# Kernel optimization log

Measured on AMD Instinct MI355X. Metric: run time of the kernel, lower is better.

The kernel has to match this reference:

```python
import jax, jax.numpy as jnp
import numpy as np

N_NODES = 8192
N_FEATURES = 512
EMB = 128
N_HEADS = 4
EPS = 1e-6


def setup_inputs() -> dict:
    key = jax.random.key(0)
    k1, k2, k3 = jax.random.split(key, 3)
    X = jax.random.normal(k1, (N_NODES, N_FEATURES), dtype=jnp.float32)
    W = jax.random.normal(k2, (N_FEATURES, EMB), dtype=jnp.float32)
    Z = jax.random.normal(k3, (N_HEADS, N_NODES, EMB), dtype=jnp.float32)
    beta = jnp.ones((), dtype=jnp.float32)
    return {"X": X, "W": W, "Z": Z, "beta": beta}


def reference(X, W, Z, beta):
    # DenseLayer: node embedding
    X_emb = X @ W                                   # [N, E]
    # AffinityLayer: Z @ X_emb^T then cosine-style normalization
    aff = jnp.einsum('hne,me->hnm', Z, X_emb)       # [H, N, N]
    X_norm = jnp.linalg.norm(X_emb, axis=-1)        # [N]
    Z_norm = jnp.linalg.norm(Z, axis=-1)            # [H, N]
    aff = aff / (X_norm[None, None, :] + EPS)
    aff = aff / (Z_norm[:, :, None] + EPS)
    # PoolingLayer: max over heads
    aff = jnp.max(aff, axis=0)                      # [N, N]
    # undirected -> symmetrize
    aff = (aff + aff.T) / 2.0
    # ScalingLayer: map [-1,1] -> [0,1]
    aff = (aff + 1.0) / 2.0
    # ExponentiationLayer
    aff = jnp.power(aff, beta)
    return aff
```

## Files before the change

kernel.cpp:

```cpp
#include <hip/hip_runtime.h>
#include <stdint.h>

#define N_NODES 8192
#define N_FEAT  512
#define EMB     128
#define N_HEADS 4
#define TILE    64
#define TGRID   (N_NODES / TILE)

typedef __attribute__((ext_vector_type(8))) short bf16x8;
typedef __attribute__((ext_vector_type(4))) float f32x4;

__device__ __forceinline__ unsigned short f2bf(float f) {
  union { float f; unsigned int u; } x; x.f = f;
  unsigned int r = (x.u + 0x7FFFu + ((x.u >> 16) & 1u)) >> 16;
  return (unsigned short)r;
}

__global__ void __launch_bounds__(256) xw_kernel(const float* __restrict__ X,
                                                 const float* __restrict__ W,
                                                 float* __restrict__ Xe) {
  __shared__ float xs[8][N_FEAT];
  const int t = threadIdx.x;
  const int row0 = blockIdx.x * 8;
#pragma unroll
  for (int i = 0; i < 16; ++i) {
    int idx = t + i * 256;
    xs[idx >> 9][idx & 511] = X[(size_t)(row0 + (idx >> 9)) * N_FEAT + (idx & 511)];
  }
  __syncthreads();
  const int j = t & 127;
  const int rh = t >> 7;
  float a0 = 0.f, a1 = 0.f, a2 = 0.f, a3 = 0.f;
  for (int k = 0; k < N_FEAT; k += 4) {
    float w0 = W[(k + 0) * EMB + j];
    float w1 = W[(k + 1) * EMB + j];
    float w2 = W[(k + 2) * EMB + j];
    float w3 = W[(k + 3) * EMB + j];
#pragma unroll
    for (int u = 0; u < 4; ++u) {
      float w = (u == 0) ? w0 : (u == 1) ? w1 : (u == 2) ? w2 : w3;
      a0 += xs[rh * 4 + 0][k + u] * w;
      a1 += xs[rh * 4 + 1][k + u] * w;
      a2 += xs[rh * 4 + 2][k + u] * w;
      a3 += xs[rh * 4 + 3][k + u] * w;
    }
  }
  Xe[(size_t)(row0 + rh * 4 + 0) * EMB + j] = a0;
  Xe[(size_t)(row0 + rh * 4 + 1) * EMB + j] = a1;
  Xe[(size_t)(row0 + rh * 4 + 2) * EMB + j] = a2;
  Xe[(size_t)(row0 + rh * 4 + 3) * EMB + j] = a3;
}

__global__ void __launch_bounds__(256) norm_kernel(const float* __restrict__ in,
                                                   unsigned short* __restrict__ out,
                                                   int nrows) {
  const int row = blockIdx.x * 4 + (threadIdx.x >> 6);
  const int lane = threadIdx.x & 63;
  if (row >= nrows) return;
  float2 v = *(const float2*)&in[(size_t)row * EMB + lane * 2];
  float ss = v.x * v.x + v.y * v.y;
#pragma unroll
  for (int off = 32; off; off >>= 1) ss += __shfl_xor(ss, off);
  const float s = 1.0f / (sqrtf(ss) + 1e-6f);
  union { unsigned short u[2]; unsigned int w; } o;
  o.u[0] = f2bf(v.x * s);
  o.u[1] = f2bf(v.y * s);
  *(unsigned int*)&out[(size_t)row * EMB + lane * 2] = o.w;
}

__device__ __forceinline__ void stage_tile(unsigned short* dst,
                                           const unsigned short* __restrict__ src,
                                           int t) {
#pragma unroll
  for (int i = 0; i < 4; ++i) {
    int ch = t + i * 256;
    int row = ch >> 4;
    int kc = ch & 15;
    uint4 v = *(const uint4*)&src[row * EMB + kc * 8];
    *(uint4*)&dst[row * EMB + ((kc ^ (row & 7)) << 3)] = v;
  }
}

__device__ __forceinline__ bf16x8 ldfrag(const unsigned short* tile, int rowbase,
                                         int kk, int lane) {
  int r = rowbase + (lane & 15);
  int kc = kk * 4 + (lane >> 4);
  return *(const bf16x8*)&tile[r * EMB + ((kc ^ (r & 7)) << 3)];
}

__global__ void __launch_bounds__(256) affinity_kernel(const unsigned short* __restrict__ Xen,
                                                       const unsigned short* __restrict__ Zn,
                                                       const float* __restrict__ betap,
                                                       float* __restrict__ out) {
  __shared__ unsigned short XA[TILE * EMB];
  __shared__ unsigned short XB[TILE * EMB];
  __shared__ unsigned short ZT[TILE * 65 * 2];
  float (*Tbuf)[65] = (float(*)[65])ZT;

  int p = blockIdx.x;
  int i = (int)(((float)(2 * TGRID + 1) -
                 sqrtf((float)((2 * TGRID + 1) * (2 * TGRID + 1) - 8 * p))) * 0.5f);
  if (i < 0) i = 0;
  if (i > TGRID - 1) i = TGRID - 1;
  while (i > 0 && i * TGRID - i * (i - 1) / 2 > p) --i;
  while ((i + 1) * TGRID - (i + 1) * i / 2 <= p) ++i;
  const int bi = i;
  const int bj = i + (p - (i * TGRID - i * (i - 1) / 2));
  const bool diag = (bi == bj);

  const int t = threadIdx.x;
  const int lane = t & 63;
  const int wid = t >> 6;
  const int wr = (wid >> 1) * 32;
  const int wc = (wid & 1) * 32;

  stage_tile(XA, Xen + (size_t)bi * TILE * EMB, t);
  stage_tile(XB, Xen + (size_t)bj * TILE * EMB, t);

  f32x4 maxI[2][2], maxJ[2][2];
#pragma unroll
  for (int mi = 0; mi < 2; ++mi)
#pragma unroll
    for (int nj = 0; nj < 2; ++nj)
#pragma unroll
      for (int q = 0; q < 4; ++q) { maxI[mi][nj][q] = -3.0e38f; maxJ[mi][nj][q] = -3.0e38f; }

  for (int h = 0; h < N_HEADS; ++h) {
    __syncthreads();
    stage_tile(ZT, Zn + ((size_t)h * N_NODES + (size_t)bi * TILE) * EMB, t);
    __syncthreads();
    {
      f32x4 acc[2][2] = {};
#pragma unroll
      for (int kk = 0; kk < 4; ++kk) {
        bf16x8 za0 = ldfrag(ZT, wr + 0, kk, lane);
        bf16x8 za1 = ldfrag(ZT, wr + 16, kk, lane);
        bf16x8 xb0 = ldfrag(XB, wc + 0, kk, lane);
        bf16x8 xb1 = ldfrag(XB, wc + 16, kk, lane);
        acc[0][0] = __builtin_amdgcn_mfma_f32_16x16x32_bf16(za0, xb0, acc[0][0], 0, 0, 0);
        acc[0][1] = __builtin_amdgcn_mfma_f32_16x16x32_bf16(za0, xb1, acc[0][1], 0, 0, 0);
        acc[1][0] = __builtin_amdgcn_mfma_f32_16x16x32_bf16(za1, xb0, acc[1][0], 0, 0, 0);
        acc[1][1] = __builtin_amdgcn_mfma_f32_16x16x32_bf16(za1, xb1, acc[1][1], 0, 0, 0);
      }
#pragma unroll
      for (int mi = 0; mi < 2; ++mi)
#pragma unroll
        for (int nj = 0; nj < 2; ++nj)
#pragma unroll
          for (int q = 0; q < 4; ++q)
            maxI[mi][nj][q] = fmaxf(maxI[mi][nj][q], acc[mi][nj][q]);
    }
    if (!diag) {
      __syncthreads();
      stage_tile(ZT, Zn + ((size_t)h * N_NODES + (size_t)bj * TILE) * EMB, t);
      __syncthreads();
      f32x4 acc[2][2] = {};
#pragma unroll
      for (int kk = 0; kk < 4; ++kk) {
        bf16x8 za0 = ldfrag(ZT, wr + 0, kk, lane);
        bf16x8 za1 = ldfrag(ZT, wr + 16, kk, lane);
        bf16x8 xa0 = ldfrag(XA, wc + 0, kk, lane);
        bf16x8 xa1 = ldfrag(XA, wc + 16, kk, lane);
        acc[0][0] = __builtin_amdgcn_mfma_f32_16x16x32_bf16(za0, xa0, acc[0][0], 0, 0, 0);
        acc[0][1] = __builtin_amdgcn_mfma_f32_16x16x32_bf16(za0, xa1, acc[0][1], 0, 0, 0);
        acc[1][0] = __builtin_amdgcn_mfma_f32_16x16x32_bf16(za1, xa0, acc[1][0], 0, 0, 0);
        acc[1][1] = __builtin_amdgcn_mfma_f32_16x16x32_bf16(za1, xa1, acc[1][1], 0, 0, 0);
      }
#pragma unroll
      for (int mi = 0; mi < 2; ++mi)
#pragma unroll
        for (int nj = 0; nj < 2; ++nj)
#pragma unroll
          for (int q = 0; q < 4; ++q)
            maxJ[mi][nj][q] = fmaxf(maxJ[mi][nj][q], acc[mi][nj][q]);
    }
  }

  __syncthreads();
#pragma unroll
  for (int mi = 0; mi < 2; ++mi)
#pragma unroll
    for (int nj = 0; nj < 2; ++nj)
#pragma unroll
      for (int q = 0; q < 4; ++q) {
        int r = wr + mi * 16 + (lane >> 4) * 4 + q;
        int c = wc + nj * 16 + (lane & 15);
        Tbuf[r][c] = diag ? maxI[mi][nj][q] : maxJ[mi][nj][q];
      }
  __syncthreads();

  const float beta = betap[0];
  const bool beta1 = (beta == 1.0f);
  float vv[2][2][4];
#pragma unroll
  for (int mi = 0; mi < 2; ++mi)
#pragma unroll
    for (int nj = 0; nj < 2; ++nj)
#pragma unroll
      for (int q = 0; q < 4; ++q) {
        int r = wr + mi * 16 + (lane >> 4) * 4 + q;
        int c = wc + nj * 16 + (lane & 15);
        float a = maxI[mi][nj][q];
        float b = Tbuf[c][r];
        float v = 0.25f * (a + b) + 0.5f;
        if (!beta1) v = powf(v, beta);
        out[(size_t)(bi * TILE + r) * N_NODES + (size_t)(bj * TILE + c)] = v;
        vv[mi][nj][q] = v;
      }

  if (!diag) {
    __syncthreads();
#pragma unroll
    for (int mi = 0; mi < 2; ++mi)
#pragma unroll
      for (int nj = 0; nj < 2; ++nj)
#pragma unroll
        for (int q = 0; q < 4; ++q) {
          int r = wr + mi * 16 + (lane >> 4) * 4 + q;
          int c = wc + nj * 16 + (lane & 15);
          Tbuf[c][r] = vv[mi][nj][q];
        }
    __syncthreads();
#pragma unroll
    for (int i2 = 0; i2 < 16; ++i2) {
      int row = (t >> 6) + i2 * 4;
      int col = t & 63;
      out[(size_t)(bj * TILE + row) * N_NODES + (size_t)(bi * TILE + col)] = Tbuf[row][col];
    }
  }
}

extern "C" void kernel_launch(void* const* d_in, const int* in_sizes, int n_in,
                              void* d_out, int out_size, void* d_ws, size_t ws_size,
                              hipStream_t stream) {
  const float* X = (const float*)d_in[0];
  const float* W = (const float*)d_in[1];
  const float* Z = (const float*)d_in[2];
  const float* beta = (const float*)d_in[3];
  float* out = (float*)d_out;
  char* ws = (char*)d_ws;

  float* Xe = (float*)ws;
  unsigned short* Xen = (unsigned short*)(ws + (4u << 20));
  unsigned short* Zn  = (unsigned short*)(ws + (6u << 20));

  hipLaunchKernelGGL(xw_kernel, dim3(N_NODES / 8), dim3(256), 0, stream, X, W, Xe);
  hipLaunchKernelGGL(norm_kernel, dim3(N_NODES / 4), dim3(256), 0, stream, Xe, Xen, N_NODES);
  hipLaunchKernelGGL(norm_kernel, dim3(N_HEADS * N_NODES / 4), dim3(256), 0, stream,
                     Z, Zn, N_HEADS * N_NODES);
  hipLaunchKernelGGL(affinity_kernel, dim3(TGRID * (TGRID + 1) / 2), dim3(256), 0, stream,
                     Xen, Zn, beta, out);
}
```

Before: 193.7 us.

## Rewrite affinity pipeline with 128-tiles, 32x32 MFMA, async double-buffered Z staging

Fuses the XW matmul with row normalization and writes X and Z embeddings in a pre-swizzled tiled bf16 layout. The affinity kernel moves to 128x128 tiles with 512 threads and 32x32x16 MFMAs, holding X fragments in registers. Z tiles are staged with global_load_lds into a double buffer so the next head's load overlaps the current compute, and block indices are interleaved across the triangle. The transpose buffer now holds bf16 values, which cuts LDS use but adds rounding to the mirrored half of the output.

```diff
diff --git a/kernel.cpp b/kernel.cpp
--- a/kernel.cpp
+++ b/kernel.cpp
@@ -1,232 +1,263 @@
 #include <hip/hip_runtime.h>
 #include <stdint.h>
+#include <stddef.h>
 
 #define N_NODES 8192
 #define N_FEAT  512
 #define EMB     128
 #define N_HEADS 4
-#define TILE    64
-#define TGRID   (N_NODES / TILE)
-
-typedef __attribute__((ext_vector_type(8))) short bf16x8;
-typedef __attribute__((ext_vector_type(4))) float f32x4;
+#define TILE    128
+#define TG      (N_NODES / TILE)
+#define NPAIR   (TG * (TG + 1) / 2)
+#define TILE_ELEMS (TILE * EMB)
+
+typedef __attribute__((ext_vector_type(8)))  short bf16x8;
+typedef __attribute__((ext_vector_type(16))) float f32x16;
 
 __device__ __forceinline__ unsigned short f2bf(float f) {
   union { float f; unsigned int u; } x; x.f = f;
   unsigned int r = (x.u + 0x7FFFu + ((x.u >> 16) & 1u)) >> 16;
   return (unsigned short)r;
 }
-
-__global__ void __launch_bounds__(256) xw_kernel(const float* __restrict__ X,
+__device__ __forceinline__ float bf2f(unsigned short u) {
+  union { unsigned int u; float f; } x; x.u = ((unsigned int)u) << 16;
+  return x.f;
+}
+
+__device__ __forceinline__ void gl_lds16(const unsigned short* g, unsigned short* l) {
+  __builtin_amdgcn_global_load_lds(
+      (__attribute__((address_space(1))) void*)(void*)g,
+      (__attribute__((address_space(3))) void*)l, 16, 0, 0);
+}
+
+__device__ __forceinline__ int swz_off(int r, int c) {
+  int kc = c >> 3;
+  return r * EMB + (((kc ^ (r & 7)) << 3) | (c & 7));
+}
+
+__device__ __forceinline__ int tidx(int r, int c) {
+  int m = (r & 31) ^ ((r & 4) << 2);
+  return r * 128 + (c ^ m);
+}
+
+__global__ void __launch_bounds__(512) xw_kernel(const float* __restrict__ X,
                                                  const float* __restrict__ W,
-                                                 float* __restrict__ Xe) {
-  __shared__ float xs[8][N_FEAT];
+                                                 unsigned short* __restrict__ Xen) {
+  __shared__ float xs[32][N_FEAT];
   const int t = threadIdx.x;
-  const int row0 = blockIdx.x * 8;
-#pragma unroll
-  for (int i = 0; i < 16; ++i) {
-    int idx = t + i * 256;
-    xs[idx >> 9][idx & 511] = X[(size_t)(row0 + (idx >> 9)) * N_FEAT + (idx & 511)];
+  const int row0 = blockIdx.x * 32;
+#pragma unroll
+  for (int i = 0; i < 8; ++i) {
+    int e4 = i * 512 + t;
+    int row = e4 >> 7;
+    int col = (e4 & 127) * 4;
+    *(float4*)&xs[row][col] = *(const float4*)&X[(size_t)(row0 + row) * N_FEAT + col];
   }
   __syncthreads();
-  const int j = t & 127;
-  const int rh = t >> 7;
-  float a0 = 0.f, a1 = 0.f, a2 = 0.f, a3 = 0.f;
-  for (int k = 0; k < N_FEAT; k += 4) {
-    float w0 = W[(k + 0) * EMB + j];
-    float w1 = W[(k + 1) * EMB + j];
-    float w2 = W[(k + 2) * EMB + j];
-    float w3 = W[(k + 3) * EMB + j];
-#pragma unroll
-    for (int u = 0; u < 4; ++u) {
-      float w = (u == 0) ? w0 : (u == 1) ? w1 : (u == 2) ? w2 : w3;
-      a0 += xs[rh * 4 + 0][k + u] * w;
-      a1 += xs[rh * 4 + 1][k + u] * w;
-      a2 += xs[rh * 4 + 2][k + u] * w;
-      a3 += xs[rh * 4 + 3][k + u] * w;
-    }
-  }
-  Xe[(size_t)(row0 + rh * 4 + 0) * EMB + j] = a0;
-  Xe[(size_t)(row0 + rh * 4 + 1) * EMB + j] = a1;
-  Xe[(size_t)(row0 + rh * 4 + 2) * EMB + j] = a2;
-  Xe[(size_t)(row0 + rh * 4 + 3) * EMB + j] = a3;
-}
-
-__global__ void __launch_bounds__(256) norm_kernel(const float* __restrict__ in,
-                                                   unsigned short* __restrict__ out,
-                                                   int nrows) {
+  const int c0 = (t & 31) * 4;
+  const int r0 = (t >> 5) * 2;
+  float a00=0.f,a01=0.f,a02=0.f,a03=0.f,a10=0.f,a11=0.f,a12=0.f,a13=0.f;
+  for (int k = 0; k < N_FEAT; k += 2) {
+    float4 w0 = *(const float4*)&W[(size_t)k * EMB + c0];
+    float4 w1 = *(const float4*)&W[(size_t)(k + 1) * EMB + c0];
+    float x00 = xs[r0][k],     x01 = xs[r0][k + 1];
+    float x10 = xs[r0 + 1][k], x11 = xs[r0 + 1][k + 1];
+    a00 += x00*w0.x; a01 += x00*w0.y; a02 += x00*w0.z; a03 += x00*w0.w;
+    a10 += x10*w0.x; a11 += x10*w0.y; a12 += x10*w0.z; a13 += x10*w0.w;
+    a00 += x01*w1.x; a01 += x01*w1.y; a02 += x01*w1.z; a03 += x01*w1.w;
+    a10 += x11*w1.x; a11 += x11*w1.y; a12 += x11*w1.z; a13 += x11*w1.w;
+  }
+  float s0 = a00*a00 + a01*a01 + a02*a02 + a03*a03;
+  float s1 = a10*a10 + a11*a11 + a12*a12 + a13*a13;
+#pragma unroll
+  for (int off = 16; off >= 1; off >>= 1) {
+    s0 += __shfl_xor(s0, off);
+    s1 += __shfl_xor(s1, off);
+  }
+  float inv0 = 1.0f / (sqrtf(s0) + 1e-6f);
+  float inv1 = 1.0f / (sqrtf(s1) + 1e-6f);
+  union { unsigned short u[4]; uint2 v; } o0, o1;
+  o0.u[0]=f2bf(a00*inv0); o0.u[1]=f2bf(a01*inv0); o0.u[2]=f2bf(a02*inv0); o0.u[3]=f2bf(a03*inv0);
+  o1.u[0]=f2bf(a10*inv1); o1.u[1]=f2bf(a11*inv1); o1.u[2]=f2bf(a12*inv1); o1.u[3]=f2bf(a13*inv1);
+  int n0 = row0 + r0;
+  int t0 = n0 >> 7, rr0 = n0 & 127;
+  int t1 = (n0 + 1) >> 7, rr1 = (n0 + 1) & 127;
+  *(uint2*)&Xen[(size_t)t0 * TILE_ELEMS + swz_off(rr0, c0)] = o0.v;
+  *(uint2*)&Xen[(size_t)t1 * TILE_ELEMS + swz_off(rr1, c0)] = o1.v;
+}
+
+__global__ void __launch_bounds__(256) znorm_kernel(const float* __restrict__ in,
+                                                    unsigned short* __restrict__ out) {
   const int row = blockIdx.x * 4 + (threadIdx.x >> 6);
   const int lane = threadIdx.x & 63;
-  if (row >= nrows) return;
   float2 v = *(const float2*)&in[(size_t)row * EMB + lane * 2];
   float ss = v.x * v.x + v.y * v.y;
 #pragma unroll
-  for (int off = 32; off; off >>= 1) ss += __shfl_xor(ss, off);
+  for (int off = 32; off >= 1; off >>= 1) ss += __shfl_xor(ss, off);
   const float s = 1.0f / (sqrtf(ss) + 1e-6f);
   union { unsigned short u[2]; unsigned int w; } o;
   o.u[0] = f2bf(v.x * s);
   o.u[1] = f2bf(v.y * s);
-  *(unsigned int*)&out[(size_t)row * EMB + lane * 2] = o.w;
-}
-
-__device__ __forceinline__ void stage_tile(unsigned short* dst,
-                                           const unsigned short* __restrict__ src,
-                                           int t) {
+  int tile = row >> 7, r = row & 127, c = lane * 2;
+  *(unsigned int*)&out[(size_t)tile * TILE_ELEMS + swz_off(r, c)] = o.w;
+}
+
+__device__ __forceinline__ void stageZ(unsigned short* dstLds, const unsigned short* src,
+                                       int wid, int lane) {
 #pragma unroll
   for (int i = 0; i < 4; ++i) {
-    int ch = t + i * 256;
-    int row = ch >> 4;
-    int kc = ch & 15;
-    uint4 v = *(const uint4*)&src[row * EMB + kc * 8];
-    *(uint4*)&dst[row * EMB + ((kc ^ (row & 7)) << 3)] = v;
-  }
-}
-
-__device__ __forceinline__ bf16x8 ldfrag(const unsigned short* tile, int rowbase,
-                                         int kk, int lane) {
-  int r = rowbase + (lane & 15);
-  int kc = kk * 4 + (lane >> 4);
-  return *(const bf16x8*)&tile[r * EMB + ((kc ^ (r & 7)) << 3)];
-}
-
-__global__ void __launch_bounds__(256) affinity_kernel(const unsigned short* __restrict__ Xen,
-                                                       const unsigned short* __restrict__ Zn,
-                                                       const float* __restrict__ betap,
-                                                       float* __restrict__ out) {
-  __shared__ unsigned short XA[TILE * EMB];
-  __shared__ unsigned short XB[TILE * EMB];
-  __shared__ unsigned short ZT[TILE * 65 * 2];
-  float (*Tbuf)[65] = (float(*)[65])ZT;
-
-  int p = blockIdx.x;
-  int i = (int)(((float)(2 * TGRID + 1) -
-                 sqrtf((float)((2 * TGRID + 1) * (2 * TGRID + 1) - 8 * p))) * 0.5f);
+    int cbase = i * 512 + wid * 64;
+    gl_lds16(src + (size_t)(cbase + lane) * 8, dstLds + (size_t)cbase * 8);
+  }
+}
+
+__device__ __forceinline__ void do_stage(const unsigned short* cur, const bf16x8 (&XB)[8],
+                                         f32x16 (&M)[2], int R0, int fr, int fh) {
+  f32x16 acc0 = {}, acc1 = {};
+  const int rb = R0 + fr;
+  const int sw = rb & 7;
+  const unsigned short* base0 = cur + rb * EMB;
+#pragma unroll
+  for (int kk = 0; kk < 8; ++kk) {
+    int kc = kk * 2 + fh;
+    int off = ((kc ^ sw) << 3);
+    bf16x8 a0 = *(const bf16x8*)(base0 + off);
+    bf16x8 a1 = *(const bf16x8*)(base0 + 32 * EMB + off);
+    acc0 = __builtin_amdgcn_mfma_f32_32x32x16_bf16(a0, XB[kk], acc0, 0, 0, 0);
+    acc1 = __builtin_amdgcn_mfma_f32_32x32x16_bf16(a1, XB[kk], acc1, 0, 0, 0);
+  }
+#pragma unroll
+  for (int q = 0; q < 16; ++q) {
+    M[0][q] = fmaxf(M[0][q], acc0[q]);
+    M[1][q] = fmaxf(M[1][q], acc1[q]);
+  }
+}
+
+__global__ void __launch_bounds__(512, 1) affinity_kernel(const unsigned short* __restrict__ Xen,
+                                                          const unsigned short* __restrict__ Zn,
+                                                          const float* __restrict__ betap,
+                                                          float* __restrict__ out) {
+  __shared__ __align__(16) unsigned short Zb[2][TILE_ELEMS];
+  unsigned short* Tb = &Zb[0][0];
+
+  int bid = blockIdx.x;
+  int p = (bid & 7) * (NPAIR / 8) + (bid >> 3);
+  int i = (int)(((float)(2 * TG + 1) -
+                 sqrtf((float)((2 * TG + 1) * (2 * TG + 1) - 8 * p))) * 0.5f);
   if (i < 0) i = 0;
-  if (i > TGRID - 1) i = TGRID - 1;
-  while (i > 0 && i * TGRID - i * (i - 1) / 2 > p) --i;
-  while ((i + 1) * TGRID - (i + 1) * i / 2 <= p) ++i;
+  if (i > TG - 1) i = TG - 1;
+  while (i > 0 && i * TG - i * (i - 1) / 2 > p) --i;
+  while ((i + 1) * TG - (i + 1) * i / 2 <= p) ++i;
   const int bi = i;
-  const int bj = i + (p - (i * TGRID - i * (i - 1) / 2));
+  const int bj = i + (p - (i * TG - i * (i - 1) / 2));
   const bool diag = (bi == bj);
+  const int NS = diag ? 4 : 8;
 
   const int t = threadIdx.x;
   const int lane = t & 63;
   const int wid = t >> 6;
-  const int wr = (wid >> 1) * 32;
-  const int wc = (wid & 1) * 32;
-
-  stage_tile(XA, Xen + (size_t)bi * TILE * EMB, t);
-  stage_tile(XB, Xen + (size_t)bj * TILE * EMB, t);
-
-  f32x4 maxI[2][2], maxJ[2][2];
-#pragma unroll
-  for (int mi = 0; mi < 2; ++mi)
-#pragma unroll
-    for (int nj = 0; nj < 2; ++nj)
-#pragma unroll
-      for (int q = 0; q < 4; ++q) { maxI[mi][nj][q] = -3.0e38f; maxJ[mi][nj][q] = -3.0e38f; }
-
-  for (int h = 0; h < N_HEADS; ++h) {
+  const int R0 = (wid >> 2) * 64;
+  const int C0 = (wid & 3) * 32;
+  const int fr = lane & 31;
+  const int fh = lane >> 5;
+
+  stageZ(Zb[0], Zn + ((size_t)(0 * TG + bi) << 14), wid, lane);
+
+  bf16x8 XjB[8], XiB[8];
+  {
+    const unsigned short* xj = Xen + ((size_t)bj << 14);
+    const int r = C0 + fr;
+    const int sw = r & 7;
+#pragma unroll
+    for (int kk = 0; kk < 8; ++kk) {
+      int kc = kk * 2 + fh;
+      XjB[kk] = *(const bf16x8*)&xj[r * EMB + ((kc ^ sw) << 3)];
+    }
+    if (!diag) {
+      const unsigned short* xi = Xen + ((size_t)bi << 14);
+#pragma unroll
+      for (int kk = 0; kk < 8; ++kk) {
+        int kc = kk * 2 + fh;
+        XiB[kk] = *(const bf16x8*)&xi[r * EMB + ((kc ^ sw) << 3)];
+      }
+    }
+  }
+
+  f32x16 maxI[2], maxJ[2];
+#pragma unroll
+  for (int q = 0; q < 16; ++q) {
+    maxI[0][q] = -3.0e38f; maxI[1][q] = -3.0e38f;
+    maxJ[0][q] = -3.0e38f; maxJ[1][q] = -3.0e38f;
+  }
+
+  __syncthreads();
+
+#pragma unroll
+  for (int s = 0; s < 4; ++s) {
+    if (s + 1 < NS) {
+      int h = (s + 1) & 3;
+      int tl = (s + 1 < 4) ? bi : bj;
+      stageZ(Zb[(s + 1) & 1], Zn + ((size_t)(h * TG + tl) << 14), wid, lane);
+    }
+    do_stage(Zb[s & 1], XjB, maxI, R0, fr, fh);
     __syncthreads();
-    stage_tile(ZT, Zn + ((size_t)h * N_NODES + (size_t)bi * TILE) * EMB, t);
-    __syncthreads();
-    {
-      f32x4 acc[2][2] = {};
-#pragma unroll
-      for (int kk = 0; kk < 4; ++kk) {
-        bf16x8 za0 = ldfrag(ZT, wr + 0, kk, lane);
-        bf16x8 za1 = ldfrag(ZT, wr + 16, kk, lane);
-        bf16x8 xb0 = ldfrag(XB, wc + 0, kk, lane);
-        bf16x8 xb1 = ldfrag(XB, wc + 16, kk, lane);
-        acc[0][0] = __builtin_amdgcn_mfma_f32_16x16x32_bf16(za0, xb0, acc[0][0], 0, 0, 0);
-        acc[0][1] = __builtin_amdgcn_mfma_f32_16x16x32_bf16(za0, xb1, acc[0][1], 0, 0, 0);
-        acc[1][0] = __builtin_amdgcn_mfma_f32_16x16x32_bf16(za1, xb0, acc[1][0], 0, 0, 0);
-        acc[1][1] = __builtin_amdgcn_mfma_f32_16x16x32_bf16(za1, xb1, acc[1][1], 0, 0, 0);
+  }
+  if (!diag) {
+#pragma unroll
+    for (int s = 4; s < 8; ++s) {
+      if (s < 7) {
+        int h = (s + 1) & 3;
+        stageZ(Zb[(s + 1) & 1], Zn + ((size_t)(h * TG + bj) << 14), wid, lane);
       }
-#pragma unroll
-      for (int mi = 0; mi < 2; ++mi)
-#pragma unroll
-        for (int nj = 0; nj < 2; ++nj)
-#pragma unroll
-          for (int q = 0; q < 4; ++q)
-            maxI[mi][nj][q] = fmaxf(maxI[mi][nj][q], acc[mi][nj][q]);
-    }
-    if (!diag) {
+      do_stage(Zb[s & 1], XiB, maxJ, R0, fr, fh);
       __syncthreads();
-      stage_tile(ZT, Zn + ((size_t)h * N_NODES + (size_t)bj * TILE) * EMB, t);
-      __syncthreads();
-      f32x4 acc[2][2] = {};
-#pragma unroll
-      for (int kk = 0; kk < 4; ++kk) {
-        bf16x8 za0 = ldfrag(ZT, wr + 0, kk, lane);
-        bf16x8 za1 = ldfrag(ZT, wr + 16, kk, lane);
-        bf16x8 xa0 = ldfrag(XA, wc + 0, kk, lane);
-        bf16x8 xa1 = ldfrag(XA, wc + 16, kk, lane);
-        acc[0][0] = __builtin_amdgcn_mfma_f32_16x16x32_bf16(za0, xa0, acc[0][0], 0, 0, 0);
-        acc[0][1] = __builtin_amdgcn_mfma_f32_16x16x32_bf16(za0, xa1, acc[0][1], 0, 0, 0);
-        acc[1][0] = __builtin_amdgcn_mfma_f32_16x16x32_bf16(za1, xa0, acc[1][0], 0, 0, 0);
-        acc[1][1] = __builtin_amdgcn_mfma_f32_16x16x32_bf16(za1, xa1, acc[1][1], 0, 0, 0);
-      }
-#pragma unroll
-      for (int mi = 0; mi < 2; ++mi)
-#pragma unroll
-        for (int nj = 0; nj < 2; ++nj)
-#pragma unroll
-          for (int q = 0; q < 4; ++q)
-            maxJ[mi][nj][q] = fmaxf(maxJ[mi][nj][q], acc[mi][nj][q]);
-    }
-  }
-
+    }
+  }
+
+#pragma unroll
+  for (int ma = 0; ma < 2; ++ma)
+#pragma unroll
+    for (int q = 0; q < 16; ++q) {
+      int r = R0 + ma * 32 + (q & 3) + 8 * (q >> 2) + 4 * fh;
+      int c = C0 + fr;
+      Tb[tidx(r, c)] = f2bf(diag ? maxI[ma][q] : maxJ[ma][q]);
+    }
   __syncthreads();
-#pragma unroll
-  for (int mi = 0; mi < 2; ++mi)
-#pragma unroll
-    for (int nj = 0; nj < 2; ++nj)
-#pragma unroll
-      for (int q = 0; q < 4; ++q) {
-        int r = wr + mi * 16 + (lane >> 4) * 4 + q;
-        int c = wc + nj * 16 + (lane & 15);
-        Tbuf[r][c] = diag ? maxI[mi][nj][q] : maxJ[mi][nj][q];
-      }
-  __syncthreads();
 
   const float beta = betap[0];
-  const bool beta1 = (beta == 1.0f);
-  float vv[2][2][4];
-#pragma unroll
-  for (int mi = 0; mi < 2; ++mi)
-#pragma unroll
-    for (int nj = 0; nj < 2; ++nj)
-#pragma unroll
-      for (int q = 0; q < 4; ++q) {
-        int r = wr + mi * 16 + (lane >> 4) * 4 + q;
-        int c = wc + nj * 16 + (lane & 15);
-        float a = maxI[mi][nj][q];
-        float b = Tbuf[c][r];
-        float v = 0.25f * (a + b) + 0.5f;
-        if (!beta1) v = powf(v, beta);
-        out[(size_t)(bi * TILE + r) * N_NODES + (size_t)(bj * TILE + c)] = v;
-        vv[mi][nj][q] = v;
-      }
+  const bool bp = (beta != 1.0f);
+  float vv[2][16];
+#pragma unroll
+  for (int ma = 0; ma < 2; ++ma)
+#pragma unroll
+    for (int q = 0; q < 16; ++q) {
+      int r = R0 + ma * 32 + (q & 3) + 8 * (q >> 2) + 4 * fh;
+      int c = C0 + fr;
+      float a = maxI[ma][q];
+      float b = bf2f(Tb[tidx(c, r)]);
+      float v = 0.25f * (a + b) + 0.5f;
+      if (bp) v = powf(v, beta);
+      out[(size_t)(bi * TILE + r) * N_NODES + (size_t)(bj * TILE + c)] = v;
+      vv[ma][q] = v;
+    }
 
   if (!diag) {
     __syncthreads();
 #pragma unroll
-    for (int mi = 0; mi < 2; ++mi)
-#pragma unroll
-      for (int nj = 0; nj < 2; ++nj)
-#pragma unroll
-        for (int q = 0; q < 4; ++q) {
-          int r = wr + mi * 16 + (lane >> 4) * 4 + q;
-          int c = wc + nj * 16 + (lane & 15);
-          Tbuf[c][r] = vv[mi][nj][q];
-        }
+    for (int ma = 0; ma < 2; ++ma)
+#pragma unroll
+      for (int q = 0; q < 16; ++q) {
+        int r = R0 + ma * 32 + (q & 3) + 8 * (q >> 2) + 4 * fh;
+        int c = C0 + fr;
+        Tb[tidx(c, r)] = f2bf(vv[ma][q]);
+      }
     __syncthreads();
 #pragma unroll
-    for (int i2 = 0; i2 < 16; ++i2) {
-      int row = (t >> 6) + i2 * 4;
-      int col = t & 63;
-      out[(size_t)(bj * TILE + row) * N_NODES + (size_t)(bi * TILE + col)] = Tbuf[row][col];
+    for (int it = 0; it < 32; ++it) {
+      int row = it * 4 + (t >> 7);
+      int col = t & 127;
+      out[(size_t)(bj * TILE + row) * N_NODES + (size_t)(bi * TILE + col)] =
+          bf2f(Tb[tidx(row, col)]);
     }
   }
 }
@@ -241,14 +272,10 @@
   float* out = (float*)d_out;
   char* ws = (char*)d_ws;
 
-  float* Xe = (float*)ws;
-  unsigned short* Xen = (unsigned short*)(ws + (4u << 20));
-  unsigned short* Zn  = (unsigned short*)(ws + (6u << 20));
-
-  hipLaunchKernelGGL(xw_kernel, dim3(N_NODES / 8), dim3(256), 0, stream, X, W, Xe);
-  hipLaunchKernelGGL(norm_kernel, dim3(N_NODES / 4), dim3(256), 0, stream, Xe, Xen, N_NODES);
-  hipLaunchKernelGGL(norm_kernel, dim3(N_HEADS * N_NODES / 4), dim3(256), 0, stream,
-                     Z, Zn, N_HEADS * N_NODES);
-  hipLaunchKernelGGL(affinity_kernel, dim3(TGRID * (TGRID + 1) / 2), dim3(256), 0, stream,
-                     Xen, Zn, beta, out);
-}
+  unsigned short* Xen = (unsigned short*)ws;
+  unsigned short* Zn  = (unsigned short*)(ws + (2u << 20));
+
+  hipLaunchKernelGGL(xw_kernel, dim3(N_NODES / 32), dim3(512), 0, stream, X, W, Xen);
+  hipLaunchKernelGGL(znorm_kernel, dim3(N_HEADS * N_NODES / 4), dim3(256), 0, stream, Z, Zn);
+  hipLaunchKernelGGL(affinity_kernel, dim3(NPAIR), dim3(512), 0, stream, Xen, Zn, beta, out);
+}
```

Result: faster. 183.0 us (-5.5%).
